# Performance work log

Hardware: AMD Instinct MI355X
Metric: run time of the kernel (lower is better)

The kernel has to match this reference:

```python
import jax, jax.numpy as jnp
import numpy as np

B, T, HID = 2, 2048, 2048
NH, NKV, HD = 16, 4, 128
GROUPS = NH // NKV

def _rotate_half(t):
    t1, t2 = jnp.split(t, 2, axis=-1)
    return jnp.concatenate([-t2, t1], axis=-1)

def _apply_rotary(t, cos, sin):
    # t: [B, H, T, D], cos/sin: [1, 1, T, D]
    return t * cos + _rotate_half(t) * sin

def setup_inputs() -> dict:
    key = jax.random.key(0)
    ks = jax.random.split(key, 6)
    x = jax.random.normal(ks[0], (B, T, HID), dtype=jnp.float32)
    # real rotary tables
    inv_freq = 1.0 / (10000.0 ** (jnp.arange(0, HD, 2, dtype=jnp.float32) / HD))
    pos = jnp.arange(T, dtype=jnp.float32)
    freqs = jnp.outer(pos, inv_freq)            # [T, D/2]
    emb = jnp.concatenate([freqs, freqs], -1)   # [T, D]
    cos = jnp.cos(emb)[None, None]              # [1,1,T,D]
    sin = jnp.sin(emb)[None, None]
    s = 0.02
    Wq = jax.random.normal(ks[1], (HID, NH * HD), dtype=jnp.float32) * s
    Wk = jax.random.normal(ks[2], (HID, NKV * HD), dtype=jnp.float32) * s
    Wv = jax.random.normal(ks[3], (HID, NKV * HD), dtype=jnp.float32) * s
    Wo = jax.random.normal(ks[4], (NH * HD, HID), dtype=jnp.float32) * s
    return {"x": x, "cos": cos, "sin": sin, "Wq": Wq, "Wk": Wk, "Wv": Wv, "Wo": Wo}

def reference(x, cos, sin, Wq, Wk, Wv, Wo):
    b, t, _ = x.shape
    q = (x @ Wq).reshape(b, t, NH, HD).transpose(0, 2, 1, 3)    # [B,NH,T,D]
    k = (x @ Wk).reshape(b, t, NKV, HD).transpose(0, 2, 1, 3)   # [B,NKV,T,D]
    v = (x @ Wv).reshape(b, t, NKV, HD).transpose(0, 2, 1, 3)
    q = _apply_rotary(q, cos, sin)
    k = _apply_rotary(k, cos, sin)
    # GQA without repeat_interleave: group q-heads by kv-head
    qg = q.reshape(b, NKV, GROUPS, t, HD)                       # [B,KV,G,T,D]
    scale = 1.0 / jnp.sqrt(jnp.float32(HD))
    scores = jnp.einsum('bkgtd,bksd->bkgts', qg, k) * scale     # [B,KV,G,T,S]
    causal = jnp.tril(jnp.ones((t, t), dtype=bool))
    scores = jnp.where(causal[None, None, None], scores, jnp.float32(-1e30))
    attn = jax.nn.softmax(scores, axis=-1)
    out = jnp.einsum('bkgts,bksd->bkgtd', attn, v)              # [B,KV,G,T,D]
    out = out.reshape(b, NH, t, HD).transpose(0, 2, 1, 3).reshape(b, t, NH * HD)
    return out @ Wo
```

## Files before the change

### kernel.cpp

```cpp
#include <hip/hip_runtime.h>
#include <hip/hip_bf16.h>
#include <cstdint>

typedef unsigned short u16;
typedef unsigned int u32;
typedef __bf16 bf16x8 __attribute__((ext_vector_type(8)));
typedef float f32x4 __attribute__((ext_vector_type(4)));

#define BDIM 2
#define TDIM 2048
#define HIDDIM 2048
#define NHEAD 16
#define NKVH 4
#define HD 128
#define MROWS (BDIM*TDIM)
#define NQKV 3072
#define KDIM 2048

#define MFMA16(a,b,c) __builtin_amdgcn_mfma_f32_16x16x32_bf16((a),(b),(c),0,0,0)

__device__ __forceinline__ u16 f2bf(float f) {
    __bf16 h = (__bf16)f;
    return __builtin_bit_cast(u16, h);
}
__device__ __forceinline__ float bf2f(u32 u) {
    u <<= 16;
    return __builtin_bit_cast(float, u);
}
__device__ __forceinline__ void gld16(const void* g, void* l) {
    __builtin_amdgcn_global_load_lds(
        (const __attribute__((address_space(1))) u32*)g,
        (__attribute__((address_space(3))) u32*)l, 16, 0, 0);
}

template<int CTRL>
__device__ __forceinline__ float dpp_rot(float x) {
    return __builtin_bit_cast(float,
        __builtin_amdgcn_update_dpp(0, __builtin_bit_cast(int, x),
                                    CTRL, 0xf, 0xf, true));
}
__device__ __forceinline__ float rowmax16(float x) {
    x = fmaxf(x, dpp_rot<0x121>(x));
    x = fmaxf(x, dpp_rot<0x122>(x));
    x = fmaxf(x, dpp_rot<0x124>(x));
    x = fmaxf(x, dpp_rot<0x128>(x));
    return x;
}
__device__ __forceinline__ float rowsum16(float x) {
    x += dpp_rot<0x121>(x);
    x += dpp_rot<0x122>(x);
    x += dpp_rot<0x124>(x);
    x += dpp_rot<0x128>(x);
    return x;
}

__global__ __launch_bounds__(256) void prep_kernel(const float* __restrict__ x,
                                                   u16* __restrict__ xb,
                                                   const float* __restrict__ Wq,
                                                   const float* __restrict__ Wk,
                                                   const float* __restrict__ Wv,
                                                   const float* __restrict__ Wo,
                                                   u16* __restrict__ Wqkvt,
                                                   u16* __restrict__ Wot) {
    __shared__ float tile[32][33];
    const int bi = blockIdx.x;
    const int tid = threadIdx.x;
    if (bi < 4096) {
        size_t i = ((size_t)bi * 256 + tid) * 8;
        float4 a = *(const float4*)(x + i);
        float4 b = *(const float4*)(x + i + 4);
        uint4 v;
        v.x = (u32)f2bf(a.x) | ((u32)f2bf(a.y) << 16);
        v.y = (u32)f2bf(a.z) | ((u32)f2bf(a.w) << 16);
        v.z = (u32)f2bf(b.x) | ((u32)f2bf(b.y) << 16);
        v.w = (u32)f2bf(b.z) | ((u32)f2bf(b.w) << 16);
        *(uint4*)(xb + i) = v;
        return;
    }
    const float* src;
    u16* dst;
    int N, n0, k0;
    if (bi < 8192) {
        int t = bi - 4096; src = Wq; dst = Wqkvt; N = 2048;
        n0 = (t & 63) * 32; k0 = (t >> 6) * 32;
    } else if (bi < 9216) {
        int t = bi - 8192; src = Wk; dst = Wqkvt + (size_t)2048 * KDIM; N = 512;
        n0 = (t & 15) * 32; k0 = (t >> 4) * 32;
    } else if (bi < 10240) {
        int t = bi - 9216; src = Wv; dst = Wqkvt + (size_t)2560 * KDIM; N = 512;
        n0 = (t & 15) * 32; k0 = (t >> 4) * 32;
    } else {
        int t = bi - 10240; src = Wo; dst = Wot; N = 2048;
        n0 = (t & 63) * 32; k0 = (t >> 6) * 32;
    }
    const int tx = tid & 31, ty = tid >> 5;
#pragma unroll
    for (int r = 0; r < 4; r++)
        tile[ty + 8*r][tx] = src[(size_t)(k0 + ty + 8*r) * N + n0 + tx];
    __syncthreads();
#pragma unroll
    for (int r = 0; r < 4; r++)
        dst[(size_t)(n0 + ty + 8*r) * KDIM + k0 + tx] = f2bf(tile[tx][ty + 8*r]);
}

template<int OUT_BF16>
__global__ void __launch_bounds__(256, 2) gemm_bt(const u16* __restrict__ A,
                                                  const u16* __restrict__ Bt,
                                                  void* __restrict__ C, int ldc) {
    __shared__ __align__(16) u16 Al[128 * 32];
    __shared__ __align__(16) u16 Bl[128 * 32];
    const int tid = threadIdx.x;
    const int lane = tid & 63;
    const int w = tid >> 6;
    const int wm = (w & 1) * 64;
    const int wn = (w >> 1) * 64;
    const int quad = lane >> 4;
    const int l15 = lane & 15;
    const size_t bm = (size_t)blockIdx.x * 128;
    const size_t bn = (size_t)blockIdx.y * 128;

    const int srow = lane >> 2;
    const int kq = (lane & 3) ^ ((lane >> 3) & 3);
    const int i0 = 2 * w, i1 = 2 * w + 1;

    const u16* ga0 = A + (bm + i0*16 + srow) * KDIM + kq * 8;
    const u16* ga1 = A + (bm + i1*16 + srow) * KDIM + kq * 8;
    const u16* gb0 = Bt + (bn + i0*16 + srow) * KDIM + kq * 8;
    const u16* gb1 = Bt + (bn + i1*16 + srow) * KDIM + kq * 8;

    const int swz = ((quad ^ ((l15 >> 1) & 3)) << 3);
    int aoff[4], boff[4];
#pragma unroll
    for (int t = 0; t < 4; t++) {
        aoff[t] = (wm + t*16 + l15) * 32 + swz;
        boff[t] = (wn + t*16 + l15) * 32 + swz;
    }

    f32x4 acc[4][4] = {};

    for (int kt = 0; kt < KDIM / 32; kt++) {
        gld16(ga0 + kt*32, &Al[i0 * 512]);
        gld16(ga1 + kt*32, &Al[i1 * 512]);
        gld16(gb0 + kt*32, &Bl[i0 * 512]);
        gld16(gb1 + kt*32, &Bl[i1 * 512]);
        __syncthreads();
        bf16x8 af[4], bfv[4];
#pragma unroll
        for (int t = 0; t < 4; t++) {
            af[t]  = *(const bf16x8*)&Al[aoff[t]];
            bfv[t] = *(const bf16x8*)&Bl[boff[t]];
        }
#pragma unroll
        for (int mt = 0; mt < 4; mt++)
#pragma unroll
            for (int nt = 0; nt < 4; nt++)
                acc[mt][nt] = MFMA16(af[mt], bfv[nt], acc[mt][nt]);
        __syncthreads();
    }

#pragma unroll
    for (int mt = 0; mt < 4; mt++) {
        size_t m0 = bm + wm + mt*16 + quad*4;
#pragma unroll
        for (int nt = 0; nt < 4; nt++) {
            size_t n = bn + wn + nt*16 + l15;
#pragma unroll
            for (int r = 0; r < 4; r++) {
                if (OUT_BF16)
                    ((u16*)C)[(m0 + r) * (size_t)ldc + n] = f2bf(acc[mt][nt][r]);
                else
                    ((float*)C)[(m0 + r) * (size_t)ldc + n] = acc[mt][nt][r];
            }
        }
    }
}

__global__ __launch_bounds__(256) void rotary_kernel(u16* __restrict__ QKV,
                                                     const float* __restrict__ cosT,
                                                     const float* __restrict__ sinT) {
    int i = blockIdx.x * 256 + threadIdx.x;
    int m = i / 320;
    int rem = i - m * 320;
    int head = rem >> 4;
    int d0 = (rem & 15) << 2;
    int t = m & (TDIM - 1);
    int col;
    float sc;
    if (head < NHEAD) {
        col = head * HD + d0;
        sc = 0.08838834764831845f * 1.4426950408889634f;
    } else {
        col = HIDDIM + (head - NHEAD) * HD + d0;
        sc = 1.0f;
    }
    u16* p0 = QKV + (size_t)m * NQKV + col;
    u16* p1 = p0 + 64;
    float4 cv = *(const float4*)(cosT + t * HD + d0);
    float4 sv = *(const float4*)(sinT + t * HD + d0);
    uint2 qa = *(const uint2*)p0;
    uint2 qb = *(const uint2*)p1;
    float f0[4] = { bf2f(qa.x & 0xffffu), bf2f(qa.x >> 16), bf2f(qa.y & 0xffffu), bf2f(qa.y >> 16) };
    float f1[4] = { bf2f(qb.x & 0xffffu), bf2f(qb.x >> 16), bf2f(qb.y & 0xffffu), bf2f(qb.y >> 16) };
    float c[4] = { cv.x, cv.y, cv.z, cv.w };
    float s[4] = { sv.x, sv.y, sv.z, sv.w };
    u16 o0[4], o1[4];
#pragma unroll
    for (int k = 0; k < 4; k++) {
        o0[k] = f2bf((f0[k] * c[k] - f1[k] * s[k]) * sc);
        o1[k] = f2bf((f1[k] * c[k] + f0[k] * s[k]) * sc);
    }
    uint2 w0, w1;
    w0.x = (u32)o0[0] | ((u32)o0[1] << 16);
    w0.y = (u32)o0[2] | ((u32)o0[3] << 16);
    w1.x = (u32)o1[0] | ((u32)o1[1] << 16);
    w1.y = (u32)o1[2] | ((u32)o1[3] << 16);
    *(uint2*)p0 = w0;
    *(uint2*)p1 = w1;
}

__global__ void __launch_bounds__(256, 2) attn_kernel(const u16* __restrict__ QKV,
                                                      u16* __restrict__ AO) {
    constexpr int LV = 72;
    constexpr int LP = 72;
    __shared__ __align__(16) u16 Kl[2][64 * 128];
    __shared__ __align__(16) u16 Vt[128 * LV];
    __shared__ __align__(16) u16 Pl[64 * LP];

    const int pa = blockIdx.x;
    const int h  = blockIdx.y;
    const int b  = blockIdx.z;
    const int kh = h >> 2;
    const int tid = threadIdx.x;
    const int lane = tid & 63;
    const int w = tid >> 6;
    const int quad = lane >> 4;
    const int l15 = lane & 15;

    const size_t rowbase = (size_t)b * TDIM;
    const u16* Qb = QKV + rowbase * NQKV + h * HD;
    const u16* Kb = QKV + rowbase * NQKV + HIDDIM + kh * HD;
    const u16* Vb = Kb + NKVH * HD;

    int krow[4], kgch[4];
#pragma unroll
    for (int i = 0; i < 4; i++) {
        krow[i] = w*16 + i*4 + quad;
        kgch[i] = l15 ^ (krow[i] & 7);
    }
    const int sp0 = tid & 31, dch0 = tid >> 5, dch1 = dch0 + 8;

#pragma unroll 1
    for (int ph = 0; ph < 2; ph++) {
        const int qt = ph ? (31 - pa) : pa;

        bf16x8 qf[4];
        {
            const u16* qr = Qb + (size_t)(qt*64 + w*16 + l15) * NQKV;
#pragma unroll
            for (int kt = 0; kt < 4; kt++)
                qf[kt] = *(const bf16x8*)(qr + kt*32 + quad*8);
        }
        f32x4 O[8] = {};
        float mrun[4], lrun[4];
#pragma unroll
        for (int r = 0; r < 4; r++) { mrun[r] = -1e30f; lrun[r] = 0.0f; }

#pragma unroll
        for (int i = 0; i < 4; i++)
            gld16(Kb + (size_t)krow[i] * NQKV + kgch[i]*8, &Kl[0][(w*16 + i*4) * 128]);
        uint4 vr0a, vr0b, vr1a, vr1b;
        {
            const u16* g0 = Vb + (size_t)(sp0*2) * NQKV + dch0*8;
            vr0a = *(const uint4*)g0;
            vr0b = *(const uint4*)(g0 + NQKV);
            const u16* g1 = Vb + (size_t)(sp0*2) * NQKV + dch1*8;
            vr1a = *(const uint4*)g1;
            vr1b = *(const uint4*)(g1 + NQKV);
        }

#pragma unroll 1
        for (int j = 0; j <= qt; j++) {
            {
                u32 ra[4] = { vr0a.x, vr0a.y, vr0a.z, vr0a.w };
                u32 rb[4] = { vr0b.x, vr0b.y, vr0b.z, vr0b.w };
                int s = sp0*2, d0 = dch0*8;
#pragma unroll
                for (int k2 = 0; k2 < 4; k2++) {
                    u32 lo = (ra[k2] & 0xffffu) | (rb[k2] << 16);
                    u32 hi = (ra[k2] >> 16) | (rb[k2] & 0xffff0000u);
                    *(u32*)&Vt[(d0 + 2*k2)     * LV + s] = lo;
                    *(u32*)&Vt[(d0 + 2*k2 + 1) * LV + s] = hi;
                }
                u32 rc[4] = { vr1a.x, vr1a.y, vr1a.z, vr1a.w };
                u32 rd[4] = { vr1b.x, vr1b.y, vr1b.z, vr1b.w };
                d0 = dch1*8;
#pragma unroll
                for (int k2 = 0; k2 < 4; k2++) {
                    u32 lo = (rc[k2] & 0xffffu) | (rd[k2] << 16);
                    u32 hi = (rc[k2] >> 16) | (rd[k2] & 0xffff0000u);
                    *(u32*)&Vt[(d0 + 2*k2)     * LV + s] = lo;
                    *(u32*)&Vt[(d0 + 2*k2 + 1) * LV + s] = hi;
                }
            }
            __syncthreads();

            if (j < qt) {
                const u16* Kbn = Kb + (size_t)(j+1) * 64 * NQKV;
                u16* kl = Kl[(j+1) & 1];
#pragma unroll
                for (int i = 0; i < 4; i++)
                    gld16(Kbn + (size_t)krow[i] * NQKV + kgch[i]*8, &kl[(w*16 + i*4) * 128]);
                const u16* Vbn = Vb + (size_t)(j+1) * 64 * NQKV;
                const u16* g0 = Vbn + (size_t)(sp0*2) * NQKV + dch0*8;
                vr0a = *(const uint4*)g0;
                vr0b = *(const uint4*)(g0 + NQKV);
                const u16* g1 = Vbn + (size_t)(sp0*2) * NQKV + dch1*8;
                vr1a = *(const uint4*)g1;
                vr1b = *(const uint4*)(g1 + NQKV);
            }

            const u16* kl = Kl[j & 1];
            f32x4 S[4] = {};
#pragma unroll
            for (int kt = 0; kt < 4; kt++) {
                int p = (kt*4 + quad) ^ (l15 & 7);
#pragma unroll
                for (int nt = 0; nt < 4; nt++) {
                    bf16x8 bfr = *(const bf16x8*)&kl[(nt*16 + l15)*128 + p*8];
                    S[nt] = MFMA16(qf[kt], bfr, S[nt]);
                }
            }

            if (j == qt) {
                int toff = w*16 + quad*4;
#pragma unroll
                for (int nt = 0; nt < 4; nt++) {
                    int scol = nt*16 + l15;
#pragma unroll
                    for (int r = 0; r < 4; r++)
                        if (scol > toff + r) S[nt][r] = -1e30f;
                }
            }

            float alpha[4];
#pragma unroll
            for (int r = 0; r < 4; r++) {
                float mx = fmaxf(fmaxf(S[0][r], S[1][r]), fmaxf(S[2][r], S[3][r]));
                mx = rowmax16(mx);
                float mnew = fmaxf(mrun[r], mx);
                float al = __builtin_amdgcn_exp2f(mrun[r] - mnew);
                mrun[r] = mnew;
                alpha[r] = al;
                float rs = 0.0f;
#pragma unroll
                for (int nt = 0; nt < 4; nt++) {
                    float p = __builtin_amdgcn_exp2f(S[nt][r] - mnew);
                    S[nt][r] = p;
                    rs += p;
                }
                rs = rowsum16(rs);
                lrun[r] = lrun[r] * al + rs;
            }
            bool need = (alpha[0] < 1.0f) | (alpha[1] < 1.0f) |
                        (alpha[2] < 1.0f) | (alpha[3] < 1.0f);
            if (__any(need)) {
#pragma unroll
                for (int nt = 0; nt < 8; nt++)
#pragma unroll
                    for (int r = 0; r < 4; r++)
                        O[nt][r] *= alpha[r];
            }

#pragma unroll
            for (int nt = 0; nt < 4; nt++)
#pragma unroll
                for (int r = 0; r < 4; r++)
                    Pl[(w*16 + quad*4 + r) * LP + nt*16 + l15] = f2bf(S[nt][r]);

#pragma unroll
            for (int kt = 0; kt < 2; kt++) {
                bf16x8 pa_f = *(const bf16x8*)&Pl[(w*16 + l15) * LP + kt*32 + quad*8];
#pragma unroll
                for (int nt = 0; nt < 8; nt++) {
                    bf16x8 bv = *(const bf16x8*)&Vt[(nt*16 + l15) * LV + kt*32 + quad*8];
                    O[nt] = MFMA16(pa_f, bv, O[nt]);
                }
            }
            __syncthreads();
        }

        float inv[4];
#pragma unroll
        for (int r = 0; r < 4; r++) inv[r] = 1.0f / lrun[r];
        size_t row0 = rowbase + qt*64 + w*16 + quad*4;
#pragma unroll
        for (int nt = 0; nt < 8; nt++) {
            size_t cix = (size_t)h * HD + nt*16 + l15;
#pragma unroll
            for (int r = 0; r < 4; r++)
                AO[(row0 + r) * HIDDIM + cix] = f2bf(O[nt][r] * inv[r]);
        }
    }
}

extern "C" void kernel_launch(void* const* d_in, const int* in_sizes, int n_in,
                              void* d_out, int out_size, void* d_ws, size_t ws_size,
                              hipStream_t stream) {
    (void)in_sizes; (void)n_in; (void)out_size; (void)ws_size;
    const float* x    = (const float*)d_in[0];
    const float* cosT = (const float*)d_in[1];
    const float* sinT = (const float*)d_in[2];
    const float* Wq   = (const float*)d_in[3];
    const float* Wk   = (const float*)d_in[4];
    const float* Wv   = (const float*)d_in[5];
    const float* Wo   = (const float*)d_in[6];

    char* ws = (char*)d_ws;
    u16* QKV   = (u16*)ws;
    u16* xb    = (u16*)(ws + (size_t)MROWS * NQKV * 2);
    u16* Wqkvt = (u16*)(ws + (size_t)MROWS * NQKV * 2 + (size_t)MROWS * HIDDIM * 2);
    u16* Wot   = Wqkvt + (size_t)NQKV * KDIM;

    prep_kernel<<<14336, 256, 0, stream>>>(x, xb, Wq, Wk, Wv, Wo, Wqkvt, Wot);
    gemm_bt<1><<<dim3(32, 24), 256, 0, stream>>>(xb, Wqkvt, QKV, NQKV);
    rotary_kernel<<<5120, 256, 0, stream>>>(QKV, cosT, sinT);
    attn_kernel<<<dim3(16, 16, 2), 256, 0, stream>>>(QKV, xb);
    gemm_bt<0><<<dim3(32, 16), 256, 0, stream>>>(xb, Wot, d_out, HIDDIM);
}
```

Baseline: 313.5 us.

## Compute transposed S in attention to keep P in registers and drop LDS staging

The attention kernel now computes S^T (K as the A operand, Q as B), so each lane holds one query row's scores. P can then be packed straight into an MFMA operand without the Pl shared-memory round trip, and the row max and sum need only two cross-lane shuffles. The V-transpose write uses a permuted column index to match the new P register layout. It also drops the paired-tile scheme in favour of one q-tile per block, launching 32x16x2 blocks in heaviest-first order with launch bounds raised to 3 blocks per CU, which trades the old load balancing for higher occupancy.

Result: slower. 357.1 us (+13.9%).

```diff
diff --git a/kernel.cpp b/kernel.cpp
--- a/kernel.cpp
+++ b/kernel.cpp
@@ -31,27 +31,6 @@
     __builtin_amdgcn_global_load_lds(
         (const __attribute__((address_space(1))) u32*)g,
         (__attribute__((address_space(3))) u32*)l, 16, 0, 0);
-}
-
-template<int CTRL>
-__device__ __forceinline__ float dpp_rot(float x) {
-    return __builtin_bit_cast(float,
-        __builtin_amdgcn_update_dpp(0, __builtin_bit_cast(int, x),
-                                    CTRL, 0xf, 0xf, true));
-}
-__device__ __forceinline__ float rowmax16(float x) {
-    x = fmaxf(x, dpp_rot<0x121>(x));
-    x = fmaxf(x, dpp_rot<0x122>(x));
-    x = fmaxf(x, dpp_rot<0x124>(x));
-    x = fmaxf(x, dpp_rot<0x128>(x));
-    return x;
-}
-__device__ __forceinline__ float rowsum16(float x) {
-    x += dpp_rot<0x121>(x);
-    x += dpp_rot<0x122>(x);
-    x += dpp_rot<0x124>(x);
-    x += dpp_rot<0x128>(x);
-    return x;
 }
 
 __global__ __launch_bounds__(256) void prep_kernel(const float* __restrict__ x,
@@ -218,15 +197,13 @@
     *(uint2*)p1 = w1;
 }
 
-__global__ void __launch_bounds__(256, 2) attn_kernel(const u16* __restrict__ QKV,
+__global__ void __launch_bounds__(256, 3) attn_kernel(const u16* __restrict__ QKV,
                                                       u16* __restrict__ AO) {
     constexpr int LV = 72;
-    constexpr int LP = 72;
     __shared__ __align__(16) u16 Kl[2][64 * 128];
     __shared__ __align__(16) u16 Vt[128 * LV];
-    __shared__ __align__(16) u16 Pl[64 * LP];
-
-    const int pa = blockIdx.x;
+
+    const int qt = 31 - blockIdx.x;
     const int h  = blockIdx.y;
     const int b  = blockIdx.z;
     const int kh = h >> 2;
@@ -248,157 +225,159 @@
         kgch[i] = l15 ^ (krow[i] & 7);
     }
     const int sp0 = tid & 31, dch0 = tid >> 5, dch1 = dch0 + 8;
+    const int s0v = sp0 * 2;
+    const int ccv = (s0v & ~0x1C) | ((s0v & 0x0C) << 1) | ((s0v & 0x10) >> 2);
+
+    bf16x8 qf[4];
+    {
+        const u16* qr = Qb + (size_t)(qt*64 + w*16 + l15) * NQKV;
+#pragma unroll
+        for (int kt = 0; kt < 4; kt++)
+            qf[kt] = *(const bf16x8*)(qr + kt*32 + quad*8);
+    }
+    f32x4 O[8] = {};
+    float mrun = -1e30f, lrun = 0.0f;
+
+#pragma unroll
+    for (int i = 0; i < 4; i++)
+        gld16(Kb + (size_t)krow[i] * NQKV + kgch[i]*8, &Kl[0][(w*16 + i*4) * 128]);
+    uint4 vr0a, vr0b, vr1a, vr1b;
+    {
+        const u16* g0 = Vb + (size_t)s0v * NQKV + dch0*8;
+        vr0a = *(const uint4*)g0;
+        vr0b = *(const uint4*)(g0 + NQKV);
+        const u16* g1 = Vb + (size_t)s0v * NQKV + dch1*8;
+        vr1a = *(const uint4*)g1;
+        vr1b = *(const uint4*)(g1 + NQKV);
+    }
 
 #pragma unroll 1
-    for (int ph = 0; ph < 2; ph++) {
-        const int qt = ph ? (31 - pa) : pa;
-
-        bf16x8 qf[4];
+    for (int j = 0; j <= qt; j++) {
         {
-            const u16* qr = Qb + (size_t)(qt*64 + w*16 + l15) * NQKV;
-#pragma unroll
-            for (int kt = 0; kt < 4; kt++)
-                qf[kt] = *(const bf16x8*)(qr + kt*32 + quad*8);
-        }
-        f32x4 O[8] = {};
-        float mrun[4], lrun[4];
-#pragma unroll
-        for (int r = 0; r < 4; r++) { mrun[r] = -1e30f; lrun[r] = 0.0f; }
-
-#pragma unroll
-        for (int i = 0; i < 4; i++)
-            gld16(Kb + (size_t)krow[i] * NQKV + kgch[i]*8, &Kl[0][(w*16 + i*4) * 128]);
-        uint4 vr0a, vr0b, vr1a, vr1b;
-        {
-            const u16* g0 = Vb + (size_t)(sp0*2) * NQKV + dch0*8;
+            u32 ra[4] = { vr0a.x, vr0a.y, vr0a.z, vr0a.w };
+            u32 rb[4] = { vr0b.x, vr0b.y, vr0b.z, vr0b.w };
+            int d0 = dch0*8;
+#pragma unroll
+            for (int k2 = 0; k2 < 4; k2++) {
+                u32 lo = (ra[k2] & 0xffffu) | (rb[k2] << 16);
+                u32 hi = (ra[k2] >> 16) | (rb[k2] & 0xffff0000u);
+                *(u32*)&Vt[(d0 + 2*k2)     * LV + ccv] = lo;
+                *(u32*)&Vt[(d0 + 2*k2 + 1) * LV + ccv] = hi;
+            }
+            u32 rc[4] = { vr1a.x, vr1a.y, vr1a.z, vr1a.w };
+            u32 rd[4] = { vr1b.x, vr1b.y, vr1b.z, vr1b.w };
+            d0 = dch1*8;
+#pragma unroll
+            for (int k2 = 0; k2 < 4; k2++) {
+                u32 lo = (rc[k2] & 0xffffu) | (rd[k2] << 16);
+                u32 hi = (rc[k2] >> 16) | (rd[k2] & 0xffff0000u);
+                *(u32*)&Vt[(d0 + 2*k2)     * LV + ccv] = lo;
+                *(u32*)&Vt[(d0 + 2*k2 + 1) * LV + ccv] = hi;
+            }
+        }
+        __syncthreads();
+
+        if (j < qt) {
+            const u16* Kbn = Kb + (size_t)(j+1) * 64 * NQKV;
+            u16* kl = Kl[(j+1) & 1];
+#pragma unroll
+            for (int i = 0; i < 4; i++)
+                gld16(Kbn + (size_t)krow[i] * NQKV + kgch[i]*8, &kl[(w*16 + i*4) * 128]);
+            const u16* Vbn = Vb + (size_t)(j+1) * 64 * NQKV;
+            const u16* g0 = Vbn + (size_t)s0v * NQKV + dch0*8;
             vr0a = *(const uint4*)g0;
             vr0b = *(const uint4*)(g0 + NQKV);
-            const u16* g1 = Vb + (size_t)(sp0*2) * NQKV + dch1*8;
+            const u16* g1 = Vbn + (size_t)s0v * NQKV + dch1*8;
             vr1a = *(const uint4*)g1;
             vr1b = *(const uint4*)(g1 + NQKV);
         }
 
-#pragma unroll 1
-        for (int j = 0; j <= qt; j++) {
-            {
-                u32 ra[4] = { vr0a.x, vr0a.y, vr0a.z, vr0a.w };
-                u32 rb[4] = { vr0b.x, vr0b.y, vr0b.z, vr0b.w };
-                int s = sp0*2, d0 = dch0*8;
-#pragma unroll
-                for (int k2 = 0; k2 < 4; k2++) {
-                    u32 lo = (ra[k2] & 0xffffu) | (rb[k2] << 16);
-                    u32 hi = (ra[k2] >> 16) | (rb[k2] & 0xffff0000u);
-                    *(u32*)&Vt[(d0 + 2*k2)     * LV + s] = lo;
-                    *(u32*)&Vt[(d0 + 2*k2 + 1) * LV + s] = hi;
+        const u16* kl = Kl[j & 1];
+        f32x4 S[4] = {};
+#pragma unroll
+        for (int kt = 0; kt < 4; kt++) {
+            int p = (kt*4 + quad) ^ (l15 & 7);
+#pragma unroll
+            for (int nt = 0; nt < 4; nt++) {
+                bf16x8 afr = *(const bf16x8*)&kl[(nt*16 + l15)*128 + p*8];
+                S[nt] = MFMA16(afr, qf[kt], S[nt]);
+            }
+        }
+
+        if (j == qt) {
+            const int qloc = w*16 + l15;
+#pragma unroll
+            for (int nt = 0; nt < 4; nt++) {
+                const int sb = nt*16 + quad*4;
+#pragma unroll
+                for (int r = 0; r < 4; r++)
+                    if (sb + r > qloc) S[nt][r] = -1e30f;
+            }
+        }
+
+        {
+            float mx0 = fmaxf(fmaxf(S[0][0], S[0][1]), fmaxf(S[0][2], S[0][3]));
+            float mx1 = fmaxf(fmaxf(S[1][0], S[1][1]), fmaxf(S[1][2], S[1][3]));
+            float mx2 = fmaxf(fmaxf(S[2][0], S[2][1]), fmaxf(S[2][2], S[2][3]));
+            float mx3 = fmaxf(fmaxf(S[3][0], S[3][1]), fmaxf(S[3][2], S[3][3]));
+            float mx = fmaxf(fmaxf(mx0, mx1), fmaxf(mx2, mx3));
+            mx = fmaxf(mx, __shfl_xor(mx, 16, 64));
+            mx = fmaxf(mx, __shfl_xor(mx, 32, 64));
+            float mnew = fmaxf(mrun, mx);
+            float alpha = __builtin_amdgcn_exp2f(mrun - mnew);
+            mrun = mnew;
+            float rs = 0.0f;
+#pragma unroll
+            for (int nt = 0; nt < 4; nt++)
+#pragma unroll
+                for (int r = 0; r < 4; r++) {
+                    float pv = __builtin_amdgcn_exp2f(S[nt][r] - mnew);
+                    S[nt][r] = pv;
+                    rs += pv;
                 }
-                u32 rc[4] = { vr1a.x, vr1a.y, vr1a.z, vr1a.w };
-                u32 rd[4] = { vr1b.x, vr1b.y, vr1b.z, vr1b.w };
-                d0 = dch1*8;
-#pragma unroll
-                for (int k2 = 0; k2 < 4; k2++) {
-                    u32 lo = (rc[k2] & 0xffffu) | (rd[k2] << 16);
-                    u32 hi = (rc[k2] >> 16) | (rd[k2] & 0xffff0000u);
-                    *(u32*)&Vt[(d0 + 2*k2)     * LV + s] = lo;
-                    *(u32*)&Vt[(d0 + 2*k2 + 1) * LV + s] = hi;
-                }
-            }
-            __syncthreads();
-
-            if (j < qt) {
-                const u16* Kbn = Kb + (size_t)(j+1) * 64 * NQKV;
-                u16* kl = Kl[(j+1) & 1];
-#pragma unroll
-                for (int i = 0; i < 4; i++)
-                    gld16(Kbn + (size_t)krow[i] * NQKV + kgch[i]*8, &kl[(w*16 + i*4) * 128]);
-                const u16* Vbn = Vb + (size_t)(j+1) * 64 * NQKV;
-                const u16* g0 = Vbn + (size_t)(sp0*2) * NQKV + dch0*8;
-                vr0a = *(const uint4*)g0;
-                vr0b = *(const uint4*)(g0 + NQKV);
-                const u16* g1 = Vbn + (size_t)(sp0*2) * NQKV + dch1*8;
-                vr1a = *(const uint4*)g1;
-                vr1b = *(const uint4*)(g1 + NQKV);
-            }
-
-            const u16* kl = Kl[j & 1];
-            f32x4 S[4] = {};
-#pragma unroll
-            for (int kt = 0; kt < 4; kt++) {
-                int p = (kt*4 + quad) ^ (l15 & 7);
-#pragma unroll
-                for (int nt = 0; nt < 4; nt++) {
-                    bf16x8 bfr = *(const bf16x8*)&kl[(nt*16 + l15)*128 + p*8];
-                    S[nt] = MFMA16(qf[kt], bfr, S[nt]);
-                }
-            }
-
-            if (j == qt) {
-                int toff = w*16 + quad*4;
-#pragma unroll
-                for (int nt = 0; nt < 4; nt++) {
-                    int scol = nt*16 + l15;
-#pragma unroll
-                    for (int r = 0; r < 4; r++)
-                        if (scol > toff + r) S[nt][r] = -1e30f;
-                }
-            }
-
-            float alpha[4];
-#pragma unroll
-            for (int r = 0; r < 4; r++) {
-                float mx = fmaxf(fmaxf(S[0][r], S[1][r]), fmaxf(S[2][r], S[3][r]));
-                mx = rowmax16(mx);
-                float mnew = fmaxf(mrun[r], mx);
-                float al = __builtin_amdgcn_exp2f(mrun[r] - mnew);
-                mrun[r] = mnew;
-                alpha[r] = al;
-                float rs = 0.0f;
-#pragma unroll
-                for (int nt = 0; nt < 4; nt++) {
-                    float p = __builtin_amdgcn_exp2f(S[nt][r] - mnew);
-                    S[nt][r] = p;
-                    rs += p;
-                }
-                rs = rowsum16(rs);
-                lrun[r] = lrun[r] * al + rs;
-            }
-            bool need = (alpha[0] < 1.0f) | (alpha[1] < 1.0f) |
-                        (alpha[2] < 1.0f) | (alpha[3] < 1.0f);
-            if (__any(need)) {
+            rs += __shfl_xor(rs, 16, 64);
+            rs += __shfl_xor(rs, 32, 64);
+            lrun = lrun * alpha + rs;
+            if (__any(alpha < 1.0f)) {
 #pragma unroll
                 for (int nt = 0; nt < 8; nt++)
-#pragma unroll
-                    for (int r = 0; r < 4; r++)
-                        O[nt][r] *= alpha[r];
-            }
-
-#pragma unroll
-            for (int nt = 0; nt < 4; nt++)
-#pragma unroll
-                for (int r = 0; r < 4; r++)
-                    Pl[(w*16 + quad*4 + r) * LP + nt*16 + l15] = f2bf(S[nt][r]);
-
-#pragma unroll
-            for (int kt = 0; kt < 2; kt++) {
-                bf16x8 pa_f = *(const bf16x8*)&Pl[(w*16 + l15) * LP + kt*32 + quad*8];
-#pragma unroll
-                for (int nt = 0; nt < 8; nt++) {
-                    bf16x8 bv = *(const bf16x8*)&Vt[(nt*16 + l15) * LV + kt*32 + quad*8];
-                    O[nt] = MFMA16(pa_f, bv, O[nt]);
-                }
-            }
-            __syncthreads();
-        }
-
-        float inv[4];
-#pragma unroll
-        for (int r = 0; r < 4; r++) inv[r] = 1.0f / lrun[r];
-        size_t row0 = rowbase + qt*64 + w*16 + quad*4;
+                    O[nt] *= alpha;
+            }
+        }
+
+        u32 c0[4], c1[4];
+#pragma unroll
+        for (int nt = 0; nt < 4; nt++) {
+            c0[nt] = (u32)f2bf(S[nt][0]) | ((u32)f2bf(S[nt][1]) << 16);
+            c1[nt] = (u32)f2bf(S[nt][2]) | ((u32)f2bf(S[nt][3]) << 16);
+        }
+#pragma unroll
+        for (int kt = 0; kt < 2; kt++) {
+            uint4 bq;
+            bq.x = c0[2*kt];
+            bq.y = c1[2*kt];
+            bq.z = c0[2*kt+1];
+            bq.w = c1[2*kt+1];
+            bf16x8 pf = __builtin_bit_cast(bf16x8, bq);
+#pragma unroll
+            for (int nt = 0; nt < 8; nt++) {
+                bf16x8 av = *(const bf16x8*)&Vt[(nt*16 + l15) * LV + kt*32 + quad*8];
+                O[nt] = MFMA16(av, pf, O[nt]);
+            }
+        }
+        __syncthreads();
+    }
+
+    {
+        float inv = 1.0f / lrun;
+        size_t row = rowbase + qt*64 + w*16 + l15;
+        u16* outp = AO + row * HIDDIM + h * HD + quad*4;
 #pragma unroll
         for (int nt = 0; nt < 8; nt++) {
-            size_t cix = (size_t)h * HD + nt*16 + l15;
-#pragma unroll
-            for (int r = 0; r < 4; r++)
-                AO[(row0 + r) * HIDDIM + cix] = f2bf(O[nt][r] * inv[r]);
+            uint2 o;
+            o.x = (u32)f2bf(O[nt][0] * inv) | ((u32)f2bf(O[nt][1] * inv) << 16);
+            o.y = (u32)f2bf(O[nt][2] * inv) | ((u32)f2bf(O[nt][3] * inv) << 16);
+            *(uint2*)(outp + nt*16) = o;
         }
     }
 }
@@ -424,6 +403,6 @@
     prep_kernel<<<14336, 256, 0, stream>>>(x, xb, Wq, Wk, Wv, Wo, Wqkvt, Wot);
     gemm_bt<1><<<dim3(32, 24), 256, 0, stream>>>(xb, Wqkvt, QKV, NQKV);
     rotary_kernel<<<5120, 256, 0, stream>>>(QKV, cosT, sinT);
-    attn_kernel<<<dim3(16, 16, 2), 256, 0, stream>>>(QKV, xb);
+    attn_kernel<<<dim3(32, 16, 2), 256, 0, stream>>>(QKV, xb);
     gemm_bt<0><<<dim3(32, 16), 256, 0, stream>>>(xb, Wot, d_out, HIDDIM);
 }
```
